# Kernel optimization log

Measured on AMD Instinct MI355X. Metric: run time of the kernel, lower is better.

The kernel has to match this reference:

```python
import jax, jax.numpy as jnp
import numpy as np

H = 2048          # hidden_size
NH = 16           # num heads
DN = 128          # nope_head_dim
DR = 64           # rope_head_dim
DQ = DN + DR      # q_head_dim = 192
DV = 128          # v_head_dim
KVR = 512         # kv_lora_rank
QR = 1536         # q_lora_rank
THETA = 100000.0
EPS = 1e-5


def rms_norm(x, w, eps=EPS):
    var = jnp.mean(x * x, axis=-1, keepdims=True)
    return w * (x * jax.lax.rsqrt(var + eps))


def rotate_half(x):
    x1, x2 = jnp.split(x, 2, axis=-1)
    return jnp.concatenate([-x2, x1], axis=-1)


def rope_cos_sin(seq_len, dim, base, dtype):
    inv_freq = 1.0 / (base ** (jnp.arange(0, dim, 2, dtype=jnp.float32) / dim))
    t = jnp.arange(seq_len, dtype=jnp.float32)
    freqs = jnp.outer(t, inv_freq)          # [S, dim/2]
    emb = jnp.concatenate([freqs, freqs], axis=-1)  # [S, dim]
    return jnp.cos(emb).astype(dtype), jnp.sin(emb).astype(dtype)


def setup_inputs() -> dict:
    key = jax.random.key(0)
    ks = jax.random.split(key, 9)
    B, S = 1, 2048
    sc = lambda fan_in: 1.0 / np.sqrt(fan_in)
    return {
        "x":           jax.random.normal(ks[0], (B, S, H), jnp.float32),
        "wq_down":     jax.random.normal(ks[1], (H, QR), jnp.float32) * sc(H),
        "q_up_norm_w": jnp.ones((QR,), jnp.float32),
        "wq_up":       jax.random.normal(ks[2], (QR, NH * DQ), jnp.float32) * sc(QR),
        "wkv_down":    jax.random.normal(ks[3], (H, KVR), jnp.float32) * sc(H),
        "kv_norm_w":   jnp.ones((KVR,), jnp.float32),
        "wk_up":       jax.random.normal(ks[4], (KVR, NH * DQ), jnp.float32) * sc(KVR),
        "wv_up":       jax.random.normal(ks[5], (KVR, NH * DV), jnp.float32) * sc(KVR),
        "wo":          jax.random.normal(ks[6], (NH * DV, H), jnp.float32) * sc(NH * DV),
    }


def reference(x, wq_down, q_up_norm_w, wq_up, wkv_down, kv_norm_w, wk_up, wv_up, wo):
    B, S, _ = x.shape
    # low-rank Q path
    q_lat = rms_norm(x @ wq_down, q_up_norm_w)
    q = (q_lat @ wq_up).reshape(B, S, NH, DQ)
    q_nope, q_pe = q[..., :DN], q[..., DN:]
    # low-rank KV path
    kv_lat = rms_norm(x @ wkv_down, kv_norm_w)
    k = (kv_lat @ wk_up).reshape(B, S, NH, DQ)
    v = (kv_lat @ wv_up).reshape(B, S, NH, DV)
    k_nope, k_pe = k[..., :DN], k[..., DN:]
    # partial RoPE on the rope dims ([B,S,NH,DR]; cos/sin broadcast over B,NH)
    cos, sin = rope_cos_sin(S, DR, THETA, x.dtype)
    cos = cos[None, :, None, :]
    sin = sin[None, :, None, :]
    q_pe = q_pe * cos + rotate_half(q_pe) * sin
    k_pe = k_pe * cos + rotate_half(k_pe) * sin
    q = jnp.concatenate([q_nope, q_pe], axis=-1)  # [B,S,NH,DQ]
    k = jnp.concatenate([k_nope, k_pe], axis=-1)
    # causal SDPA, scale = 1/sqrt(q_head_dim)
    scale = 1.0 / np.sqrt(DQ)
    scores = jnp.einsum("bqhd,bkhd->bhqk", q, k) * scale
    causal = jnp.tril(jnp.ones((S, S), dtype=bool))
    scores = jnp.where(causal[None, None], scores, jnp.finfo(scores.dtype).min)
    probs = jax.nn.softmax(scores, axis=-1)
    out = jnp.einsum("bhqk,bkhd->bqhd", probs, v).reshape(B, S, NH * DV)
    return out @ wo
```

## Files before the change

### kernel.cpp

```cpp
#include <hip/hip_runtime.h>
#include <math.h>

typedef unsigned short u16;
typedef short s16x4 __attribute__((ext_vector_type(4)));
typedef short s16x8 __attribute__((ext_vector_type(8)));
typedef __bf16 bf16x8 __attribute__((ext_vector_type(8)));
typedef float f32x4 __attribute__((ext_vector_type(4)));

#define S_LEN 2048
#define NHEAD 16
#define QCOLS 3072
#define VCOLS 2048
#define ATT_SCALE 0.07216878364870323f

__device__ __forceinline__ u16 f2bf(float f) {
    unsigned u = __float_as_uint(f);
    u += 0x7fffu + ((u >> 16) & 1u);
    return (u16)(u >> 16);
}
__device__ __forceinline__ float bf2f(u16 h) {
    return __uint_as_float(((unsigned)h) << 16);
}

typedef const __attribute__((address_space(1))) void gas_void;
typedef __attribute__((address_space(3))) void las_void;
__device__ __forceinline__ void gload_lds16(const void* g, void* l) {
    __builtin_amdgcn_global_load_lds(
        (gas_void*)(unsigned long long)g,
        (las_void*)(unsigned)(unsigned long long)l, 16, 0, 0);
}

template<int BM, int BN, int OMODE>
__global__ __launch_bounds__(256) void gemm_bf16(
    const u16* __restrict__ A, const u16* __restrict__ Bt,
    void* __restrict__ Cv, int M, int N, int K,
    const float* __restrict__ cost, const float* __restrict__ sint,
    u16* __restrict__ Cv2)
{
    constexpr int BK = 64;
    __shared__ u16 As[2][BM * BK];
    __shared__ u16 Bs[2][BN * BK];
    const int t = threadIdx.x;
    const int lane = t & 63, wid = t >> 6;
    const int wr = wid >> 1, wc = wid & 1;
    const int g = lane >> 4, cl = lane & 15;
    const size_t bm = (size_t)blockIdx.y * BM;
    const size_t bn = (size_t)blockIdx.x * BN;
    constexpr int MR = BM / 32, NR = BN / 32;
    constexpr int APW = BM * BK * 2 / 1024 / 4;
    constexpr int BPW = BN * BK * 2 / 1024 / 4;

    auto stage = [&](int buf, int k0) {
#pragma unroll
        for (int i = 0; i < APW; ++i) {
            int rnd = wid * APW + i;
            int fb  = (rnd << 10) + (lane << 4);
            int row = fb >> 7;
            int ke  = (fb & 127) >> 1;
            gload_lds16(A + (bm + row) * K + k0 + ke, (char*)As[buf] + (rnd << 10));
        }
#pragma unroll
        for (int i = 0; i < BPW; ++i) {
            int rnd = wid * BPW + i;
            int fb  = (rnd << 10) + (lane << 4);
            int row = fb >> 7;
            int ke  = (fb & 127) >> 1;
            gload_lds16(Bt + (bn + row) * K + k0 + ke, (char*)Bs[buf] + (rnd << 10));
        }
    };

    f32x4 acc[MR][NR] = {};
    stage(0, 0);
    int cur = 0;
    for (int k0 = 0; k0 < K; k0 += BK) {
        __syncthreads();
        if (k0 + BK < K) stage(cur ^ 1, k0 + BK);
#pragma unroll
        for (int ks = 0; ks < 2; ++ks) {
            s16x8 av[MR], bv[NR];
#pragma unroll
            for (int m = 0; m < MR; ++m)
                av[m] = *(const s16x8*)((const char*)As[cur] +
                        (wr*(BM/2) + m*16 + cl) * 128 + ks*64 + g*16);
#pragma unroll
            for (int n = 0; n < NR; ++n)
                bv[n] = *(const s16x8*)((const char*)Bs[cur] +
                        (wc*(BN/2) + n*16 + cl) * 128 + ks*64 + g*16);
#pragma unroll
            for (int m = 0; m < MR; ++m)
#pragma unroll
                for (int n = 0; n < NR; ++n)
                    acc[m][n] = __builtin_amdgcn_mfma_f32_16x16x32_bf16(
                        __builtin_bit_cast(bf16x8, av[m]),
                        __builtin_bit_cast(bf16x8, bv[n]), acc[m][n], 0, 0, 0);
        }
        cur ^= 1;
    }

    if constexpr (OMODE == 3 || OMODE == 4) {
        const int band = ((int)(bn >> 6)) + wc;
        u16* C = (u16*)Cv;
        if (OMODE == 4 && band >= 48) {
#pragma unroll
            for (int m = 0; m < MR; ++m)
#pragma unroll
                for (int n = 0; n < NR; ++n) {
                    size_t vcol = bn + wc*(BN/2) + n*16 + cl - 3072;
#pragma unroll
                    for (int j = 0; j < 4; ++j) {
                        size_t row = bm + wr*(BM/2) + m*16 + g*4 + j;
                        Cv2[vcol * M + row] = f2bf(acc[m][n][j]);
                    }
                }
        } else {
            const bool pe = (band % 3) == 2;
            const int NN = 3072;
#pragma unroll
            for (int m = 0; m < MR; ++m) {
                const size_t rbase = bm + wr*(BM/2) + m*16 + g*4;
                if (pe) {
#pragma unroll
                    for (int n = 0; n < 2; ++n) {
                        const int j = n*16 + cl;
                        const size_t colA = bn + wc*(BN/2) + n*16 + cl;
#pragma unroll
                        for (int jj = 0; jj < 4; ++jj) {
                            const size_t r = rbase + jj;
                            float co = cost[r*32 + j], sn = sint[r*32 + j];
                            float a = acc[m][n][jj], b = acc[m][n+2][jj];
                            C[r*NN + colA]      = f2bf(a*co - b*sn);
                            C[r*NN + colA + 32] = f2bf(b*co + a*sn);
                        }
                    }
                } else {
#pragma unroll
                    for (int n = 0; n < NR; ++n) {
                        const size_t col = bn + wc*(BN/2) + n*16 + cl;
#pragma unroll
                        for (int jj = 0; jj < 4; ++jj)
                            C[(rbase + jj)*NN + col] = f2bf(acc[m][n][jj]);
                    }
                }
            }
        }
    } else {
#pragma unroll
        for (int m = 0; m < MR; ++m)
#pragma unroll
            for (int n = 0; n < NR; ++n) {
                size_t col = bn + wc*(BN/2) + n*16 + cl;
#pragma unroll
                for (int j = 0; j < 4; ++j) {
                    size_t row = bm + wr*(BM/2) + m*16 + g*4 + j;
                    if constexpr (OMODE == 0)
                        ((float*)Cv)[row * N + col] = acc[m][n][j];
                    else if constexpr (OMODE == 1)
                        ((u16*)Cv)[row * N + col] = f2bf(acc[m][n][j]);
                    else
                        ((u16*)Cv)[col * M + row] = f2bf(acc[m][n][j]);
                }
            }
    }
}

__global__ __launch_bounds__(256) void transpose_cast5(
    const float* __restrict__ w0, u16* __restrict__ o0,
    const float* __restrict__ w1, u16* __restrict__ o1,
    const float* __restrict__ w2, u16* __restrict__ o2,
    const float* __restrict__ w3, u16* __restrict__ o3,
    const float* __restrict__ w4, u16* __restrict__ o4)
{
    const int z = blockIdx.z;
    const float* in; u16* out; int K, N;
    if      (z == 0) { in = w0; out = o0; K = 2048; N = 1536; }
    else if (z == 1) { in = w1; out = o1; K = 2048; N = 512;  }
    else if (z == 2) { in = w2; out = o2; K = 1536; N = 3072; }
    else if (z == 3) { in = w3; out = o3; K = 512;  N = 3072; }
    else             { in = w4; out = o4; K = 512;  N = 2048; }
    const int bn = blockIdx.x * 32, bk = blockIdx.y * 32;
    if (bn >= N || bk >= K) return;

    __shared__ float tile[32][33];
    const int tx = threadIdx.x & 31, ty = threadIdx.x >> 5;
#pragma unroll
    for (int r = 0; r < 32; r += 8)
        tile[ty + r][tx] = in[(size_t)(bk + ty + r) * N + bn + tx];
    __syncthreads();
#pragma unroll
    for (int r = 0; r < 32; r += 8)
        out[(size_t)(bn + ty + r) * K + bk + tx] = f2bf(tile[tx][ty + r]);
}

__global__ __launch_bounds__(256) void transpose_cast(
    const float* __restrict__ in, u16* __restrict__ out, int K, int N)
{
    __shared__ float tile[32][33];
    const int bk = blockIdx.y * 32, bn = blockIdx.x * 32;
    const int tx = threadIdx.x & 31, ty = threadIdx.x >> 5;
#pragma unroll
    for (int r = 0; r < 32; r += 8)
        tile[ty + r][tx] = in[(size_t)(bk + ty + r) * N + bn + tx];
    __syncthreads();
#pragma unroll
    for (int r = 0; r < 32; r += 8)
        out[(size_t)(bn + ty + r) * K + bk + tx] = f2bf(tile[tx][ty + r]);
}

__global__ __launch_bounds__(256) void cast_f32_bf16(
    const float* __restrict__ in, u16* __restrict__ out, long n)
{
    long i = ((long)blockIdx.x * 256 + threadIdx.x) * 4;
    if (i >= n) return;
    f32x4 v = *(const f32x4*)(in + i);
    ushort4 q;
    q.x = f2bf(v[0]); q.y = f2bf(v[1]); q.z = f2bf(v[2]); q.w = f2bf(v[3]);
    *(ushort4*)(out + i) = q;
}

__global__ __launch_bounds__(256) void rmsnorm2(
    u16* __restrict__ qb, const float* __restrict__ qw,
    u16* __restrict__ kvb, const float* __restrict__ kvw)
{
    const int r = blockIdx.x;
    u16* buf; const float* w; int N; float invN;
    if (r < 2048) { buf = qb + (size_t)r * 1536; w = qw; N = 1536; invN = 1.f/1536.f; }
    else { buf = kvb + (size_t)(r - 2048) * 512; w = kvw; N = 512; invN = 1.f/512.f; }
    const int t = threadIdx.x;

    float ss = 0.f;
    for (int i = t * 8; i < N; i += 2048) {
        s16x8 v = *(const s16x8*)&buf[i];
#pragma unroll
        for (int e = 0; e < 8; ++e) { float f = bf2f((u16)v[e]); ss += f * f; }
    }
#pragma unroll
    for (int off = 32; off > 0; off >>= 1) ss += __shfl_down(ss, off, 64);
    __shared__ float red[4];
    __shared__ float sinv;
    if ((t & 63) == 0) red[t >> 6] = ss;
    __syncthreads();
    if (t == 0) sinv = rsqrtf((red[0]+red[1]+red[2]+red[3]) * invN + 1e-5f);
    __syncthreads();
    const float si = sinv;
    for (int i = t * 8; i < N; i += 2048) {
        s16x8 v = *(const s16x8*)&buf[i];
        s16x8 o;
#pragma unroll
        for (int e = 0; e < 8; ++e)
            o[e] = (short)f2bf(bf2f((u16)v[e]) * w[i + e] * si);
        *(s16x8*)&buf[i] = o;
    }
}

__global__ __launch_bounds__(256) void rope_table_k(
    float* __restrict__ cost, float* __restrict__ sint)
{
    int idx = blockIdx.x * 256 + threadIdx.x;
    int tp = idx >> 5, j = idx & 31;
    float invf = powf(100000.0f, -(float)j * (1.0f / 32.0f));
    float fr = (float)tp * invf;
    cost[idx] = cosf(fr);
    sint[idx] = sinf(fr);
}

__global__ __launch_bounds__(256) void attn_mfma(
    const u16* __restrict__ qg, const u16* __restrict__ kg,
    const u16* __restrict__ vtg, u16* __restrict__ og)
{
    __shared__ u16 Ks[2][64 * 192];
    __shared__ u16 VTs[128 * 64];
    __shared__ u16 Ps[4][16 * 64];

    const int t = threadIdx.x, lane = t & 63, wid = t >> 6;
    const int g = lane >> 4, cl = lane & 15;
    const int h = blockIdx.y;
    const int bx = blockIdx.x;
    const int qt = (bx & 1) ? (31 - (bx >> 1)) : (bx >> 1);
    const int qbase = qt * 64;
    const int wrow = wid * 16;

    s16x8 qv[6];
    {
        const u16* qrow = qg + (size_t)(qbase + wrow + cl) * QCOLS + h * 192;
#pragma unroll
        for (int s = 0; s < 6; ++s)
            qv[s] = *(const s16x8*)(qrow + s * 32 + g * 8);
    }

    float mreg = -1e30f, lreg = 0.f;
    f32x4 accO[8] = {};
    char* pw = (char*)Ps[wid];

    const char* kh = (const char*)(kg + (size_t)h * 192);
    const char* vh = (const char*)(vtg + (size_t)(h * 128) * S_LEN);

    auto stageK = [&](int kt2, int buf) {
        const char* ksrc = kh + (size_t)(kt2 * 64) * (QCOLS * 2);
#pragma unroll
        for (int i = 0; i < 6; ++i) {
            int rnd = wid * 6 + i;
            int fb  = (rnd << 10) + (lane << 4);
            int row = fb / 384;
            int cb  = fb - row * 384;
            gload_lds16(ksrc + (size_t)row * (QCOLS * 2) + (cb ^ ((row & 7) << 4)),
                        (char*)Ks + buf * 24576 + (rnd << 10));
        }
    };
    auto stageV = [&](int kt2) {
        const char* vsrc = vh + (size_t)(kt2 * 64) * 2;
#pragma unroll
        for (int i = 0; i < 4; ++i) {
            int rnd = wid * 4 + i;
            int fb  = (rnd << 10) + (lane << 4);
            int dv  = fb >> 7;
            int cb  = fb & 127;
            gload_lds16(vsrc + (size_t)dv * (S_LEN * 2) + (cb ^ ((dv & 7) << 4)),
                        (char*)VTs + (rnd << 10));
        }
    };

    stageK(0, 0);
    asm volatile("s_waitcnt vmcnt(0)" ::: "memory");
    __builtin_amdgcn_s_barrier();

    int cur = 0;
    for (int kt = 0; kt <= qt; ++kt) {
        const int kbase = kt * 64;
        stageV(kt);
        if (kt < qt) stageK(kt + 1, cur ^ 1);

        f32x4 accS[4] = {};
        const char* kbuf = (const char*)Ks + cur * 24576;
        __builtin_amdgcn_s_setprio(1);
#pragma unroll
        for (int n = 0; n < 4; ++n) {
            const int kvrow = n * 16 + cl;
            const char* krow = kbuf + kvrow * 384;
            const int sw = (kvrow & 7) << 4;
#pragma unroll
            for (int s = 0; s < 6; ++s) {
                s16x8 kv8 = *(const s16x8*)(krow + ((s * 64 + g * 16) ^ sw));
                accS[n] = __builtin_amdgcn_mfma_f32_16x16x32_bf16(
                    __builtin_bit_cast(bf16x8, kv8),
                    __builtin_bit_cast(bf16x8, qv[s]), accS[n], 0, 0, 0);
            }
        }
        __builtin_amdgcn_s_setprio(0);

        const int qrow_g = qbase + wrow + cl;
        float pm[4][4];
        float mx = -1e30f;
#pragma unroll
        for (int n = 0; n < 4; ++n)
#pragma unroll
            for (int j = 0; j < 4; ++j) {
                int kcol = kbase + n * 16 + g * 4 + j;
                float s = accS[n][j] * ATT_SCALE;
                s = (kcol <= qrow_g) ? s : -1e30f;
                pm[n][j] = s;
                mx = fmaxf(mx, s);
            }
        mx = fmaxf(mx, __shfl_xor(mx, 16, 64));
        mx = fmaxf(mx, __shfl_xor(mx, 32, 64));
        float mnew = fmaxf(mreg, mx);
        float c = __expf(mreg - mnew);
        float rs = 0.f;
#pragma unroll
        for (int n = 0; n < 4; ++n)
#pragma unroll
            for (int j = 0; j < 4; ++j) {
                float p = __expf(pm[n][j] - mnew);
                pm[n][j] = p;
                rs += p;
            }
        rs += __shfl_xor(rs, 16, 64);
        rs += __shfl_xor(rs, 32, 64);
        lreg = lreg * c + rs;
        mreg = mnew;

#pragma unroll
        for (int n = 0; n < 4; ++n) {
            s16x4 pk;
#pragma unroll
            for (int j = 0; j < 4; ++j) pk[j] = (short)f2bf(pm[n][j]);
            int byte = (cl * 128 + n * 32 + g * 8) ^ ((cl & 7) << 4);
            *(s16x4*)(pw + byte) = pk;
        }

        if (kt < qt) { asm volatile("s_waitcnt vmcnt(6)" ::: "memory"); }
        else         { asm volatile("s_waitcnt vmcnt(0)" ::: "memory"); }
        __builtin_amdgcn_sched_barrier(0);
        __builtin_amdgcn_s_barrier();

        float cj[4];
#pragma unroll
        for (int j = 0; j < 4; ++j) cj[j] = __shfl(c, g * 4 + j, 64);
#pragma unroll
        for (int nb = 0; nb < 8; ++nb)
#pragma unroll
            for (int j = 0; j < 4; ++j) accO[nb][j] *= cj[j];

        __builtin_amdgcn_s_setprio(1);
#pragma unroll
        for (int ks = 0; ks < 2; ++ks) {
            s16x8 pa = *(const s16x8*)(pw +
                ((cl * 128 + ks * 64 + g * 16) ^ ((cl & 7) << 4)));
#pragma unroll
            for (int nb = 0; nb < 8; ++nb) {
                s16x8 vb = *(const s16x8*)((const char*)VTs +
                    (((nb * 16 + cl) * 128 + ks * 64 + g * 16) ^ ((cl & 7) << 4)));
                accO[nb] = __builtin_amdgcn_mfma_f32_16x16x32_bf16(
                    __builtin_bit_cast(bf16x8, pa),
                    __builtin_bit_cast(bf16x8, vb), accO[nb], 0, 0, 0);
            }
        }
        __builtin_amdgcn_s_setprio(0);

        asm volatile("s_waitcnt vmcnt(0)" ::: "memory");
        __builtin_amdgcn_sched_barrier(0);
        __builtin_amdgcn_s_barrier();
        cur ^= 1;
    }

    float li[4];
#pragma unroll
    for (int j = 0; j < 4; ++j) li[j] = 1.f / __shfl(lreg, g * 4 + j, 64);
#pragma unroll
    for (int j = 0; j < 4; ++j) {
        u16* orow = og + (size_t)(qbase + wrow + g * 4 + j) * VCOLS + h * 128;
#pragma unroll
        for (int nb = 0; nb < 8; ++nb)
            orow[nb * 16 + cl] = f2bf(accO[nb][j] * li[j]);
    }
}

extern "C" void kernel_launch(void* const* d_in, const int* in_sizes, int n_in,
                              void* d_out, int out_size, void* d_ws, size_t ws_size,
                              hipStream_t stream)
{
    const float* x         = (const float*)d_in[0];
    const float* wq_down   = (const float*)d_in[1];
    const float* q_norm_w  = (const float*)d_in[2];
    const float* wq_up     = (const float*)d_in[3];
    const float* wkv_down  = (const float*)d_in[4];
    const float* kv_norm_w = (const float*)d_in[5];
    const float* wk_up     = (const float*)d_in[6];
    const float* wv_up     = (const float*)d_in[7];
    const float* wo        = (const float*)d_in[8];
    float* out = (float*)d_out;
    char* ws = (char*)d_ws;

    u16*  WQD_T  = (u16*)(ws + 0);
    u16*  WKVD_T = (u16*)(ws + 6291456);
    u16*  WKU_T  = (u16*)(ws + 8388608);
    u16*  WVU_T  = (u16*)(ws + 11534336);
    u16*  WQU_T  = (u16*)(ws + 13631488);
    u16*  XBF    = (u16*)(ws + 23068672);
    u16*  VTBUF  = (u16*)(ws + 31457280);
    u16*  QLATB  = (u16*)(ws + 48234496);
    u16*  KVLATB = (u16*)(ws + 54525952);
    u16*  QBUF   = (u16*)(ws + 56623104);
    u16*  KBUF   = (u16*)(ws + 69206016);
    float* COST  = (float*)(ws + 81788928);
    float* SINT  = (float*)(ws + 82051072);
    u16*  WO_T   = (u16*)(ws + 0);
    u16*  ATTNO  = (u16*)(ws + 23068672);

    transpose_cast5<<<dim3(96, 64, 5), 256, 0, stream>>>(
        wq_down, WQD_T, wkv_down, WKVD_T, wq_up, WQU_T, wk_up, WKU_T, wv_up, WVU_T);
    cast_f32_bf16<<<4096, 256, 0, stream>>>(x, XBF, (long)S_LEN * 2048);
    rope_table_k<<<256, 256, 0, stream>>>(COST, SINT);

    gemm_bf16<128,128,1><<<dim3(12, 16), 256, 0, stream>>>(
        XBF, WQD_T,  QLATB,  2048, 1536, 2048, nullptr, nullptr, nullptr);
    gemm_bf16< 64, 64,1><<<dim3( 8, 32), 256, 0, stream>>>(
        XBF, WKVD_T, KVLATB, 2048,  512, 2048, nullptr, nullptr, nullptr);
    rmsnorm2<<<4096, 256, 0, stream>>>(QLATB, q_norm_w, KVLATB, kv_norm_w);
    transpose_cast<<<dim3(64, 64), 256, 0, stream>>>(wo, WO_T, 2048, 2048);

    gemm_bf16<128,128,3><<<dim3(24, 16), 256, 0, stream>>>(
        QLATB,  WQU_T, QBUF, 2048, 3072, 1536, COST, SINT, nullptr);
    gemm_bf16<128,128,4><<<dim3(40, 16), 256, 0, stream>>>(
        KVLATB, WKU_T, KBUF, 2048, 5120, 512,  COST, SINT, VTBUF);

    attn_mfma<<<dim3(32, 16), 256, 0, stream>>>(QBUF, KBUF, VTBUF, ATTNO);
    gemm_bf16<128,128,0><<<dim3(16, 16), 256, 0, stream>>>(
        ATTNO, WO_T, out, 2048, 2048, 2048, nullptr, nullptr, nullptr);
}
```

Before: 353.7 us.

## Deepen GEMM pipeline to 4 stages, fuse down-projections, vectorize transposes

Reworks the bf16 GEMM mainloop into a 4-buffer, BK=32 software pipeline with explicit vmcnt waits, raw barriers and raised wave priority during MFMA, to hide global-to-LDS latency. It fuses the Q and KV down-projection GEMMs into a single launch by treating the adjacent transposed weights as one 2048-column matrix, with a new output mode that splits columns into two buffers. Weight transpose-cast kernels move to 64x64 tiles with float4 loads and ushort4 stores. The hardcoded vmcnt literals assume exactly four loads per stage and K divisible by BK with at least three tiles.

```diff
diff --git a/kernel.cpp b/kernel.cpp
--- a/kernel.cpp
+++ b/kernel.cpp
@@ -37,9 +37,9 @@
     const float* __restrict__ cost, const float* __restrict__ sint,
     u16* __restrict__ Cv2)
 {
-    constexpr int BK = 64;
-    __shared__ u16 As[2][BM * BK];
-    __shared__ u16 Bs[2][BN * BK];
+    constexpr int BK = 32;
+    __shared__ u16 As[4][BM * BK];
+    __shared__ u16 Bs[4][BN * BK];
     const int t = threadIdx.x;
     const int lane = t & 63, wid = t >> 6;
     const int wr = wid >> 1, wc = wid & 1;
@@ -49,53 +49,67 @@
     constexpr int MR = BM / 32, NR = BN / 32;
     constexpr int APW = BM * BK * 2 / 1024 / 4;
     constexpr int BPW = BN * BK * 2 / 1024 / 4;
-
-    auto stage = [&](int buf, int k0) {
+    static_assert(APW + BPW == 4, "LPW must be 4 (vmcnt literals 8/4/0)");
+
+    auto stage = [&](int s, int ti) {
+        const int k0 = ti * BK;
 #pragma unroll
         for (int i = 0; i < APW; ++i) {
             int rnd = wid * APW + i;
             int fb  = (rnd << 10) + (lane << 4);
-            int row = fb >> 7;
-            int ke  = (fb & 127) >> 1;
-            gload_lds16(A + (bm + row) * K + k0 + ke, (char*)As[buf] + (rnd << 10));
+            int row = fb >> 6;
+            int ke  = (fb & 63) >> 1;
+            gload_lds16(A + (bm + row) * K + k0 + ke, (char*)As[s] + (rnd << 10));
         }
 #pragma unroll
         for (int i = 0; i < BPW; ++i) {
             int rnd = wid * BPW + i;
             int fb  = (rnd << 10) + (lane << 4);
-            int row = fb >> 7;
-            int ke  = (fb & 127) >> 1;
-            gload_lds16(Bt + (bn + row) * K + k0 + ke, (char*)Bs[buf] + (rnd << 10));
+            int row = fb >> 6;
+            int ke  = (fb & 63) >> 1;
+            gload_lds16(Bt + (bn + row) * K + k0 + ke, (char*)Bs[s] + (rnd << 10));
         }
     };
 
     f32x4 acc[MR][NR] = {};
-    stage(0, 0);
-    int cur = 0;
-    for (int k0 = 0; k0 < K; k0 += BK) {
-        __syncthreads();
-        if (k0 + BK < K) stage(cur ^ 1, k0 + BK);
-#pragma unroll
-        for (int ks = 0; ks < 2; ++ks) {
-            s16x8 av[MR], bv[NR];
-#pragma unroll
-            for (int m = 0; m < MR; ++m)
-                av[m] = *(const s16x8*)((const char*)As[cur] +
-                        (wr*(BM/2) + m*16 + cl) * 128 + ks*64 + g*16);
+    auto compute = [&](int s) {
+        s16x8 av[MR], bv[NR];
+#pragma unroll
+        for (int m = 0; m < MR; ++m)
+            av[m] = *(const s16x8*)((const char*)As[s] +
+                    (wr*(BM/2) + m*16 + cl) * 64 + g*16);
+#pragma unroll
+        for (int n = 0; n < NR; ++n)
+            bv[n] = *(const s16x8*)((const char*)Bs[s] +
+                    (wc*(BN/2) + n*16 + cl) * 64 + g*16);
+        __builtin_amdgcn_s_setprio(1);
+#pragma unroll
+        for (int m = 0; m < MR; ++m)
 #pragma unroll
             for (int n = 0; n < NR; ++n)
-                bv[n] = *(const s16x8*)((const char*)Bs[cur] +
-                        (wc*(BN/2) + n*16 + cl) * 128 + ks*64 + g*16);
-#pragma unroll
-            for (int m = 0; m < MR; ++m)
-#pragma unroll
-                for (int n = 0; n < NR; ++n)
-                    acc[m][n] = __builtin_amdgcn_mfma_f32_16x16x32_bf16(
-                        __builtin_bit_cast(bf16x8, av[m]),
-                        __builtin_bit_cast(bf16x8, bv[n]), acc[m][n], 0, 0, 0);
-        }
-        cur ^= 1;
-    }
+                acc[m][n] = __builtin_amdgcn_mfma_f32_16x16x32_bf16(
+                    __builtin_bit_cast(bf16x8, av[m]),
+                    __builtin_bit_cast(bf16x8, bv[n]), acc[m][n], 0, 0, 0);
+        __builtin_amdgcn_s_setprio(0);
+    };
+
+    const int nt = K / BK;
+    stage(0, 0); stage(1, 1); stage(2, 2);
+    for (int ti = 0; ti < nt - 2; ++ti) {
+        asm volatile("s_waitcnt vmcnt(8)" ::: "memory");
+        __builtin_amdgcn_sched_barrier(0);
+        __builtin_amdgcn_s_barrier();
+        if (ti + 3 < nt) stage((ti + 3) & 3, ti + 3);
+        compute(ti & 3);
+    }
+    asm volatile("s_waitcnt vmcnt(4)" ::: "memory");
+    __builtin_amdgcn_sched_barrier(0);
+    __builtin_amdgcn_s_barrier();
+    compute((nt - 2) & 3);
+    asm volatile("s_waitcnt vmcnt(0)" ::: "memory");
+    __builtin_amdgcn_sched_barrier(0);
+    __builtin_amdgcn_s_barrier();
+    compute((nt - 1) & 3);
 
     if constexpr (OMODE == 3 || OMODE == 4) {
         const int band = ((int)(bn >> 6)) + wc;
@@ -143,6 +157,22 @@
                 }
             }
         }
+    } else if constexpr (OMODE == 5) {
+        const bool isq = (bn < 1536);
+        u16* base = isq ? (u16*)Cv : Cv2;
+        const size_t stride = isq ? 1536 : 512;
+        const size_t cof = isq ? 0 : 1536;
+#pragma unroll
+        for (int m = 0; m < MR; ++m)
+#pragma unroll
+            for (int n = 0; n < NR; ++n) {
+                size_t col = bn + wc*(BN/2) + n*16 + cl - cof;
+#pragma unroll
+                for (int j = 0; j < 4; ++j) {
+                    size_t row = bm + wr*(BM/2) + m*16 + g*4 + j;
+                    base[row * stride + col] = f2bf(acc[m][n][j]);
+                }
+            }
     } else {
 #pragma unroll
         for (int m = 0; m < MR; ++m)
@@ -163,7 +193,30 @@
     }
 }
 
-__global__ __launch_bounds__(256) void transpose_cast5(
+__device__ __forceinline__ void tc_body(
+    const float* __restrict__ in, u16* __restrict__ out, int K, int N,
+    int bk, int bn, int tid)
+{
+    __shared__ float tile[64][65];
+    const int tx = tid & 15, ty = tid >> 4;
+#pragma unroll
+    for (int r0 = 0; r0 < 4; ++r0)
+        *(float4*)&tile[ty + r0*16][tx*4] =
+            *(const float4*)&in[(size_t)(bk + ty + r0*16) * N + bn + tx*4];
+    __syncthreads();
+#pragma unroll
+    for (int r0 = 0; r0 < 4; ++r0) {
+        const int nn = ty + r0*16;
+        ushort4 o;
+        o.x = f2bf(tile[tx*4+0][nn]);
+        o.y = f2bf(tile[tx*4+1][nn]);
+        o.z = f2bf(tile[tx*4+2][nn]);
+        o.w = f2bf(tile[tx*4+3][nn]);
+        *(ushort4*)&out[(size_t)(bn + nn) * K + bk + tx*4] = o;
+    }
+}
+
+__global__ __launch_bounds__(256) void transpose_cast5v(
     const float* __restrict__ w0, u16* __restrict__ o0,
     const float* __restrict__ w1, u16* __restrict__ o1,
     const float* __restrict__ w2, u16* __restrict__ o2,
@@ -177,33 +230,15 @@
     else if (z == 2) { in = w2; out = o2; K = 1536; N = 3072; }
     else if (z == 3) { in = w3; out = o3; K = 512;  N = 3072; }
     else             { in = w4; out = o4; K = 512;  N = 2048; }
-    const int bn = blockIdx.x * 32, bk = blockIdx.y * 32;
+    const int bn = blockIdx.x * 64, bk = blockIdx.y * 64;
     if (bn >= N || bk >= K) return;
-
-    __shared__ float tile[32][33];
-    const int tx = threadIdx.x & 31, ty = threadIdx.x >> 5;
-#pragma unroll
-    for (int r = 0; r < 32; r += 8)
-        tile[ty + r][tx] = in[(size_t)(bk + ty + r) * N + bn + tx];
-    __syncthreads();
-#pragma unroll
-    for (int r = 0; r < 32; r += 8)
-        out[(size_t)(bn + ty + r) * K + bk + tx] = f2bf(tile[tx][ty + r]);
-}
-
-__global__ __launch_bounds__(256) void transpose_cast(
+    tc_body(in, out, K, N, bk, bn, threadIdx.x);
+}
+
+__global__ __launch_bounds__(256) void transpose_cast_v(
     const float* __restrict__ in, u16* __restrict__ out, int K, int N)
 {
-    __shared__ float tile[32][33];
-    const int bk = blockIdx.y * 32, bn = blockIdx.x * 32;
-    const int tx = threadIdx.x & 31, ty = threadIdx.x >> 5;
-#pragma unroll
-    for (int r = 0; r < 32; r += 8)
-        tile[ty + r][tx] = in[(size_t)(bk + ty + r) * N + bn + tx];
-    __syncthreads();
-#pragma unroll
-    for (int r = 0; r < 32; r += 8)
-        out[(size_t)(bn + ty + r) * K + bk + tx] = f2bf(tile[tx][ty + r]);
+    tc_body(in, out, K, N, blockIdx.y * 64, blockIdx.x * 64, threadIdx.x);
 }
 
 __global__ __launch_bounds__(256) void cast_f32_bf16(
@@ -466,17 +501,15 @@
     u16*  WO_T   = (u16*)(ws + 0);
     u16*  ATTNO  = (u16*)(ws + 23068672);
 
-    transpose_cast5<<<dim3(96, 64, 5), 256, 0, stream>>>(
+    transpose_cast5v<<<dim3(48, 32, 5), 256, 0, stream>>>(
         wq_down, WQD_T, wkv_down, WKVD_T, wq_up, WQU_T, wk_up, WKU_T, wv_up, WVU_T);
     cast_f32_bf16<<<4096, 256, 0, stream>>>(x, XBF, (long)S_LEN * 2048);
     rope_table_k<<<256, 256, 0, stream>>>(COST, SINT);
 
-    gemm_bf16<128,128,1><<<dim3(12, 16), 256, 0, stream>>>(
-        XBF, WQD_T,  QLATB,  2048, 1536, 2048, nullptr, nullptr, nullptr);
-    gemm_bf16< 64, 64,1><<<dim3( 8, 32), 256, 0, stream>>>(
-        XBF, WKVD_T, KVLATB, 2048,  512, 2048, nullptr, nullptr, nullptr);
+    gemm_bf16<128,128,5><<<dim3(16, 16), 256, 0, stream>>>(
+        XBF, WQD_T, QLATB, 2048, 2048, 2048, nullptr, nullptr, KVLATB);
     rmsnorm2<<<4096, 256, 0, stream>>>(QLATB, q_norm_w, KVLATB, kv_norm_w);
-    transpose_cast<<<dim3(64, 64), 256, 0, stream>>>(wo, WO_T, 2048, 2048);
+    transpose_cast_v<<<dim3(32, 32), 256, 0, stream>>>(wo, WO_T, 2048, 2048);
 
     gemm_bf16<128,128,3><<<dim3(24, 16), 256, 0, stream>>>(
         QLATB,  WQU_T, QBUF, 2048, 3072, 1536, COST, SINT, nullptr);
```

After: 323.2 us. -8.6%, faster.
